# Performance work log

Hardware: AMD Instinct MI355X
Metric: run time of the kernel (lower is better)

Reference implementation:

```python
import jax, jax.numpy as jnp
import numpy as np

DIM = 768
NUM_HEADS = 12
HEAD_DIM = DIM // NUM_HEADS
SCALE = HEAD_DIM ** (-0.5)
WH, WW = 14, 14
NUM_EXTRA = 1
NUM_REL_DIST = (2 * WH - 1) * (2 * WW - 1) + NUM_EXTRA * (NUM_EXTRA + 2)  # 732
N_TOK = WH * WW + NUM_EXTRA  # 197
BATCH = 64


def make_rel_pos_index():
    # mirrors the torch buffer construction (meshgrid 'ij')
    coords = np.stack(np.meshgrid(np.arange(WH), np.arange(WW), indexing='ij'))  # [2,Wh,Ww]
    coords_flat = coords.reshape(2, -1)  # [2, Wh*Ww]
    rel = coords_flat[:, :, None] - coords_flat[:, None, :]  # [2, M, M]
    rel = rel.transpose(1, 2, 0).astype(np.int64)  # [M, M, 2]
    rel[:, :, 0] += WH - 1
    rel[:, :, 1] += WW - 1
    rel[:, :, 0] *= 2 * WW - 1
    idx = np.zeros((N_TOK, N_TOK), dtype=np.int64)
    idx[NUM_EXTRA:, NUM_EXTRA:] = rel.sum(-1)
    idx[0, 0:] = NUM_REL_DIST - 3
    idx[0:, 0] = NUM_REL_DIST - 2
    idx[0, 0] = NUM_REL_DIST - 1
    return jnp.asarray(idx, dtype=jnp.int32)


def setup_inputs() -> dict:
    key = jax.random.key(0)
    ks = jax.random.split(key, 7)
    x = jax.random.normal(ks[0], (BATCH, N_TOK, DIM), dtype=jnp.float32)
    qkv_w = jax.random.normal(ks[1], (3 * DIM, DIM), dtype=jnp.float32) * (DIM ** -0.5)
    q_bias = jax.random.normal(ks[2], (DIM,), dtype=jnp.float32) * 0.02
    v_bias = jax.random.normal(ks[3], (DIM,), dtype=jnp.float32) * 0.02
    rpb_table = jax.random.normal(ks[4], (NUM_REL_DIST, NUM_HEADS), dtype=jnp.float32) * 0.02
    proj_w = jax.random.normal(ks[5], (DIM, DIM), dtype=jnp.float32) * (DIM ** -0.5)
    proj_b = jax.random.normal(ks[6], (DIM,), dtype=jnp.float32) * 0.02
    rel_index = make_rel_pos_index()
    return {"x": x, "qkv_w": qkv_w, "q_bias": q_bias, "v_bias": v_bias,
            "rpb_table": rpb_table, "proj_w": proj_w, "proj_b": proj_b,
            "rel_index": rel_index}


def reference(x, qkv_w, q_bias, v_bias, rpb_table, proj_w, proj_b, rel_index):
    B, N, C = x.shape
    # qkv bias: [q_bias, zeros, v_bias]
    qkv_bias = jnp.concatenate([q_bias, jnp.zeros_like(v_bias), v_bias]).astype(x.dtype)
    qkv = x @ qkv_w.T + qkv_bias  # [B,N,3C]
    qkv = qkv.reshape(B, N, 3, NUM_HEADS, HEAD_DIM).transpose(2, 0, 3, 1, 4)  # [3,B,H,N,d]
    q, k, v = qkv[0] * SCALE, qkv[1], qkv[2]
    # fp32 scores, as in the original
    attn = jnp.einsum('bhnd,bhmd->bhnm', q.astype(jnp.float32), k.astype(jnp.float32))
    # relative position bias gather: [N,N,H] -> [H,N,N]
    bias = rpb_table[rel_index.reshape(-1)].reshape(N, N, NUM_HEADS).transpose(2, 0, 1)
    attn = jax.nn.softmax(attn + bias[None].astype(jnp.float32), axis=-1)
    out = jnp.einsum('bhnm,bhmd->bhnd', attn, v.astype(attn.dtype))
    out = out.transpose(0, 2, 1, 3).reshape(B, N, -1).astype(x.dtype)
    return out @ proj_w.T + proj_b
```

## Files before the change

kernel.cpp:

```cpp
#include <hip/hip_runtime.h>
#include <hip/hip_bf16.h>

#define DIM 768
#define NHEADS 12
#define HD 64
#define NTOK 197
#define BATCH 64
#define NTOKENS (BATCH*NTOK)
#define NPAIR (NTOK*NTOK)
#define QK_SCALE_E2 0.18033688011f
#define LOG2E 1.44269504089f
#define CDIM 2304

typedef short bf16x8 __attribute__((ext_vector_type(8)));
typedef float f32x4 __attribute__((ext_vector_type(4)));

#define MFMA(a,b,c) __builtin_amdgcn_mfma_f32_16x16x32_bf16(a,b,c,0,0,0)

__device__ __forceinline__ unsigned short f2bf(float f) {
    union { float f; unsigned u; } v; v.f = f;
    unsigned r = v.u + 0x7FFFu + ((v.u >> 16) & 1u);
    return (unsigned short)(r >> 16);
}

__device__ __forceinline__ float bf2f(unsigned short u) {
    union { unsigned v; float f; } x; x.v = ((unsigned)u) << 16; return x.f;
}

__device__ __forceinline__ float fexp2(float x) {
    float d;
    asm("v_exp_f32 %0, %1" : "=v"(d) : "v"(x));
    return d;
}

__device__ __forceinline__ unsigned cvtpk(float lo, float hi) {
    unsigned d;
    asm("v_cvt_pk_bf16_f32 %0, %1, %2" : "=v"(d) : "v"(lo), "v"(hi));
    return d;
}

__device__ __forceinline__ unsigned vperm(unsigned s0, unsigned s1, unsigned sel) {
    unsigned d;
    asm("v_perm_b32 %0, %1, %2, %3" : "=v"(d) : "v"(s0), "v"(s1), "s"(sel));
    return d;
}

__device__ __forceinline__ void gload16(const unsigned short* g, unsigned short* l) {
    __builtin_amdgcn_global_load_lds(
        (const __attribute__((address_space(1))) void*)g,
        (__attribute__((address_space(3))) void*)l, 16, 0, 0);
}

__device__ __forceinline__ int xcd_swz(int orig, int nwg) {
    int q = nwg >> 3, r = nwg & 7;
    int xcd = orig & 7, idx = orig >> 3;
    return (xcd < r ? xcd * (q + 1) : r * (q + 1) + (xcd - r) * q) + idx;
}

#define NB_X 4728
#define NB_WQ 864
#define NB_WP 288
#define NB_BIAS 1820

__device__ __forceinline__ void cvt8(const float* __restrict__ s,
                                     unsigned short* __restrict__ d, int t, int n8) {
    if (t >= n8) return;
    float4 a = ((const float4*)s)[t * 2], b = ((const float4*)s)[t * 2 + 1];
    union { unsigned short u[8]; bf16x8 v; } p;
    p.u[0] = f2bf(a.x); p.u[1] = f2bf(a.y); p.u[2] = f2bf(a.z); p.u[3] = f2bf(a.w);
    p.u[4] = f2bf(b.x); p.u[5] = f2bf(b.y); p.u[6] = f2bf(b.z); p.u[7] = f2bf(b.w);
    ((bf16x8*)d)[t] = p.v;
}

__global__ __launch_bounds__(256) void prep(
    const float* __restrict__ x, const float* __restrict__ qw,
    const float* __restrict__ pw, const float* __restrict__ rpb,
    const int* __restrict__ rel,
    unsigned short* __restrict__ Xb, unsigned short* __restrict__ Wqb,
    unsigned short* __restrict__ Wpb, unsigned short* __restrict__ biasm)
{
    int bid = blockIdx.x;
    if (bid < NB_X) {
        cvt8(x, Xb, bid * 256 + threadIdx.x, NB_X * 256);
    } else if (bid < NB_X + NB_WQ) {
        cvt8(qw, Wqb, (bid - NB_X) * 256 + threadIdx.x, NB_WQ * 256);
    } else if (bid < NB_X + NB_WQ + NB_WP) {
        cvt8(pw, Wpb, (bid - NB_X - NB_WQ) * 256 + threadIdx.x, NB_WP * 256);
    } else {
        int t = (bid - NB_X - NB_WQ - NB_WP) * 256 + threadIdx.x;
        if (t < NHEADS * NPAIR) {
            int h = t / NPAIR, p = t - h * NPAIR;
            biasm[t] = f2bf(rpb[rel[p] * NHEADS + h] * LOG2E);
        }
    }
}

__global__ __launch_bounds__(256, 2) void gemm_qkv256(
    const unsigned short* __restrict__ Xb, const unsigned short* __restrict__ Wb,
    const float* __restrict__ qbias, const float* __restrict__ vbias,
    unsigned short* __restrict__ QKVb)
{
    __shared__ __attribute__((aligned(16))) unsigned short As[256 * 64];
    __shared__ __attribute__((aligned(16))) unsigned short Bs[128 * 64];
    int tid = threadIdx.x, lane = tid & 63, wid = tid >> 6;
    int wg = xcd_swz(blockIdx.x, 900);
    int bx = wg / 18, by = wg % 18;
    int m0 = bx * 256, n0 = by * 128;
    int wm = (wid >> 1) * 128, wn = (wid & 1) * 64;
    int r15 = lane & 15, hi = lane >> 4, sx = lane & 7;
    int sl0 = hi ^ sx, sl1 = (hi + 4) ^ sx;

    int slot8 = ((lane & 7) ^ (lane >> 3)) * 8;
    unsigned asrc[8];
    #pragma unroll
    for (int i = 0; i < 8; ++i) {
        int row = i * 32 + wid * 8 + (lane >> 3);
        int ar = m0 + row; if (ar >= NTOKENS) ar = NTOKENS - 1;
        asrc[i] = (unsigned)(ar * DIM + slot8);
    }
    unsigned bsrc[4];
    #pragma unroll
    for (int i = 0; i < 4; ++i) {
        int row = i * 32 + wid * 8 + (lane >> 3);
        bsrc[i] = (unsigned)((n0 + row) * DIM + slot8);
    }

    f32x4 acc[8][4];
    #pragma unroll
    for (int i = 0; i < 8; ++i)
        #pragma unroll
        for (int j = 0; j < 4; ++j) acc[i][j] = (f32x4){0.f, 0.f, 0.f, 0.f};

    for (int k0 = 0; k0 < DIM; k0 += 64) {
        __syncthreads();
        #pragma unroll
        for (int i = 0; i < 8; ++i)
            gload16(Xb + asrc[i] + k0, &As[i * 2048 + wid * 512 + lane * 8]);
        #pragma unroll
        for (int i = 0; i < 4; ++i)
            gload16(Wb + bsrc[i] + k0, &Bs[i * 2048 + wid * 512 + lane * 8]);
        __syncthreads();
        #pragma unroll
        for (int ks = 0; ks < 2; ++ks) {
            int so = (ks ? sl1 : sl0) * 8;
            bf16x8 af[8], bw[4];
            #pragma unroll
            for (int i = 0; i < 8; ++i)
                af[i] = *(const bf16x8*)&As[(wm + i * 16 + r15) * 64 + so];
            #pragma unroll
            for (int j = 0; j < 4; ++j)
                bw[j] = *(const bf16x8*)&Bs[(wn + j * 16 + r15) * 64 + so];
            __builtin_amdgcn_s_setprio(1);
            #pragma unroll
            for (int i = 0; i < 8; ++i)
                #pragma unroll
                for (int j = 0; j < 4; ++j)
                    acc[i][j] = MFMA(af[i], bw[j], acc[i][j]);
            __builtin_amdgcn_s_setprio(0);
        }
    }
    __syncthreads();

    unsigned short* reg = &As[wid * 4096];
    int which = n0 / DIM;
    float scl = (which == 0) ? QK_SCALE_E2 : 1.f;
    #pragma unroll
    for (int h = 0; h < 2; ++h) {
        #pragma unroll
        for (int j = 0; j < 4; ++j) {
            int colr = n0 - which * DIM + wn + j * 16 + r15;
            float bv = (which == 0) ? qbias[colr] : (which == 2 ? vbias[colr] : 0.f);
            #pragma unroll
            for (int mi = 0; mi < 4; ++mi) {
                #pragma unroll
                for (int r = 0; r < 4; ++r) {
                    int lr = mi * 16 + hi * 4 + r;
                    int c = j * 16 + r15;
                    reg[lr * 64 + (c ^ (((lr >> 2) & 3) << 4))] =
                        f2bf((acc[h * 4 + mi][j][r] + bv) * scl);
                }
            }
        }
        #pragma unroll
        for (int it = 0; it < 8; ++it) {
            int c = it * 64 + lane;
            int lr = c >> 3, cc = c & 7;
            int row = m0 + wm + h * 64 + lr;
            if (row < NTOKENS) {
                bf16x8 v = *(bf16x8*)&reg[lr * 64 + ((cc * 8) ^ (((lr >> 2) & 3) << 4))];
                *(bf16x8*)(QKVb + (size_t)row * CDIM + n0 + wn + cc * 8) = v;
            }
        }
    }
}

__global__ __launch_bounds__(256, 2) void gemm_proj(
    const unsigned short* __restrict__ Ob, const unsigned short* __restrict__ Wp,
    const float* __restrict__ pbias, float* __restrict__ out)
{
    __shared__ __attribute__((aligned(16))) unsigned short As[128 * 64];
    __shared__ __attribute__((aligned(16))) unsigned short Bs[128 * 64];
    int tid = threadIdx.x, lane = tid & 63, wid = tid >> 6;
    int wg = xcd_swz(blockIdx.x, 594);
    int bx = wg / 6, by = wg % 6;
    int m0 = bx * 128, n0 = by * 128;
    int wm = (wid >> 1) * 64, wn = (wid & 1) * 64;

    size_t abase[4], bbase[4];
    unsigned short *alds[4], *blds[4];
    #pragma unroll
    for (int i = 0; i < 4; ++i) {
        int chunk = i * 4 + wid;
        int row = chunk * 8 + (lane >> 3);
        int slot = (lane & 7) ^ (row & 7);
        int ar = m0 + row; if (ar >= NTOKENS) ar = NTOKENS - 1;
        abase[i] = (size_t)ar * DIM + slot * 8;
        bbase[i] = (size_t)(n0 + row) * DIM + slot * 8;
        alds[i] = &As[chunk * 512];
        blds[i] = &Bs[chunk * 512];
    }
    int r15 = lane & 15, hi = lane >> 4, sx = lane & 7;
    int s0 = (hi ^ sx) * 8, s1 = ((hi + 4) ^ sx) * 8;
    int arow[4], brow[4];
    #pragma unroll
    for (int i = 0; i < 4; ++i) {
        arow[i] = (wm + i * 16 + r15) * 64;
        brow[i] = (wn + i * 16 + r15) * 64;
    }

    f32x4 acc[4][4];
    #pragma unroll
    for (int i = 0; i < 4; ++i)
        #pragma unroll
        for (int j = 0; j < 4; ++j) acc[i][j] = (f32x4){0.f, 0.f, 0.f, 0.f};

    for (int k0 = 0; k0 < DIM; k0 += 64) {
        __syncthreads();
        #pragma unroll
        for (int i = 0; i < 4; ++i) {
            gload16(Ob + abase[i] + k0, alds[i]);
            gload16(Wp + bbase[i] + k0, blds[i]);
        }
        __syncthreads();
        #pragma unroll
        for (int ks = 0; ks < 2; ++ks) {
            int so = ks ? s1 : s0;
            bf16x8 af[4], bwv[4];
            #pragma unroll
            for (int i = 0; i < 4; ++i) af[i] = *(bf16x8*)&As[arow[i] + so];
            #pragma unroll
            for (int j = 0; j < 4; ++j) bwv[j] = *(bf16x8*)&Bs[brow[j] + so];
            __builtin_amdgcn_s_setprio(1);
            #pragma unroll
            for (int i = 0; i < 4; ++i)
                #pragma unroll
                for (int j = 0; j < 4; ++j)
                    acc[i][j] = MFMA(af[i], bwv[j], acc[i][j]);
            __builtin_amdgcn_s_setprio(0);
        }
    }

    #pragma unroll
    for (int j = 0; j < 4; ++j) {
        int col = n0 + wn + j * 16 + r15;
        float bv = pbias[col];
        #pragma unroll
        for (int i = 0; i < 4; ++i) {
            #pragma unroll
            for (int r = 0; r < 4; ++r) {
                int row = m0 + wm + i * 16 + hi * 4 + r;
                if (row < NTOKENS)
                    out[(size_t)row * DIM + col] = acc[i][j][r] + bv;
            }
        }
    }
}

#define KP 72
#define PP 232
#define VPITCH 256

__global__ __launch_bounds__(256, 2) void attn(
    const unsigned short* __restrict__ QKV, const unsigned short* __restrict__ biasm,
    unsigned short* __restrict__ O)
{
    __shared__ __attribute__((aligned(16))) unsigned short VT[64 * VPITCH];
    __shared__ __attribute__((aligned(16))) unsigned short KlPl[208 * KP];

    int tid = threadIdx.x, lane = tid & 63, wid = tid >> 6;
    int r15 = lane & 15, hi = lane >> 4;
    int wg = blockIdx.x;
    int g = wg >> 5, qt = (wg >> 3) & 3, p = wg & 7;
    int bh = g * 8 + p;
    int h = bh % NHEADS, b = bh / NHEADS;
    size_t tb = (size_t)b * NTOK;
    int hq = h * 64;
    int rbase = qt * 64 + wid * 16 + hi * 4;

    int kcol = (tid & 7) * 8;
    bf16x8 kreg[7];
    #pragma unroll
    for (int t = 0; t < 7; ++t) {
        int row = t * 32 + (tid >> 3);
        int rc = row < NTOK ? row : (NTOK - 1);
        kreg[t] = *(const bf16x8*)(QKV + (tb + rc) * CDIM + 768 + hq + kcol);
    }

    bf16x8 v0r[4], v1r[4];
    #pragma unroll
    for (int it = 0; it < 4; ++it) {
        int c = it * 256 + tid;
        int rp = c >> 3, kc = c & 7;
        int r0 = 2 * rp, r1 = 2 * rp + 1;
        bf16x8 z = (bf16x8)(short)0;
        v0r[it] = z; v1r[it] = z;
        if (r0 < NTOK) v0r[it] = *(const bf16x8*)(QKV + (tb + r0) * CDIM + 1536 + hq + kc * 8);
        if (r1 < NTOK) v1r[it] = *(const bf16x8*)(QKV + (tb + r1) * CDIM + 1536 + hq + kc * 8);
    }

    int qrow_g = qt * 64 + wid * 16 + r15;
    int qsrc = qrow_g < NTOK ? qrow_g : (NTOK - 1);
    bf16x8 aq[2];
    #pragma unroll
    for (int ks = 0; ks < 2; ++ks)
        aq[ks] = *(const bf16x8*)(QKV + (tb + qsrc) * CDIM + hq + ks * 32 + hi * 8);

    unsigned short breg[4][13];
    {
        const unsigned short* bb = biasm + h * NPAIR;
        #pragma unroll
        for (int r = 0; r < 4; ++r) {
            int row_g = rbase + r;
            int rowc = row_g < NTOK ? row_g : (NTOK - 1);
            const unsigned short* brow = bb + rowc * NTOK + r15;
            #pragma unroll
            for (int t = 0; t < 13; ++t) {
                int off = t * 16;
                if (t == 12 && r15 >= 5) off = 0;
                breg[r][t] = brow[off];
            }
        }
    }

    #pragma unroll
    for (int t = 0; t < 7; ++t) {
        int row = t * 32 + (tid >> 3);
        if (row < NTOK)
            *(bf16x8*)&KlPl[row * KP + kcol] = kreg[t];
    }

    #pragma unroll
    for (int it = 0; it < 4; ++it) {
        int c = it * 256 + tid;
        int rp = c >> 3, kc = c & 7;
        if (rp < 112) {
            union { bf16x8 v; unsigned u[4]; } a0, a1;
            a0.v = v0r[it]; a1.v = v1r[it];
            #pragma unroll
            for (int rr = 0; rr < 4; ++rr) {
                unsigned we = vperm(a1.u[rr], a0.u[rr], 0x05040100u);
                unsigned wo = vperm(a1.u[rr], a0.u[rr], 0x07060302u);
                int j0 = 2 * rr, j1 = 2 * rr + 1;
                int s20 = (rp >> 2) ^ j0 ^ kc;
                int s21 = (rp >> 2) ^ j1 ^ kc;
                *(unsigned*)&VT[(kc * 8 + j0) * VPITCH + s20 * 8 + (rp & 3) * 2] = we;
                *(unsigned*)&VT[(kc * 8 + j1) * VPITCH + s21 * 8 + (rp & 3) * 2] = wo;
            }
        }
    }
    __syncthreads();

    f32x4 sa[13];
    #pragma unroll
    for (int t = 0; t < 13; ++t) sa[t] = (f32x4){0.f,0.f,0.f,0.f};
    __builtin_amdgcn_s_setprio(1);
    #pragma unroll
    for (int t = 0; t < 13; ++t) {
        #pragma unroll
        for (int ks = 0; ks < 2; ++ks) {
            bf16x8 bk = *(bf16x8*)&KlPl[(t * 16 + r15) * KP + ks * 32 + hi * 8];
            sa[t] = MFMA(aq[ks], bk, sa[t]);
        }
    }
    __builtin_amdgcn_s_setprio(0);
    __syncthreads();

    int plbase = wid * (16 * PP);
    float invr[4];
    #pragma unroll
    for (int r = 0; r < 4; ++r) {
        #pragma unroll
        for (int t = 0; t < 13; ++t) {
            int col = t * 16 + r15;
            if (col < NTOK) sa[t][r] += bf2f(breg[r][t]);
            else            sa[t][r] = -1e30f;
        }
        float m0a = fmaxf(fmaxf(sa[0][r], sa[1][r]), fmaxf(sa[2][r], sa[3][r]));
        float m1a = fmaxf(fmaxf(sa[4][r], sa[5][r]), fmaxf(sa[6][r], sa[7][r]));
        float m2a = fmaxf(fmaxf(sa[8][r], sa[9][r]), fmaxf(sa[10][r], sa[11][r]));
        float mx = fmaxf(fmaxf(m0a, m1a), fmaxf(m2a, sa[12][r]));
        #pragma unroll
        for (int m = 1; m < 16; m <<= 1) mx = fmaxf(mx, __shfl_xor(mx, m));
        #pragma unroll
        for (int t = 0; t < 13; ++t)
            sa[t][r] = fexp2(sa[t][r] - mx);
        float s0a = (sa[0][r] + sa[1][r]) + (sa[2][r] + sa[3][r]);
        float s1a = (sa[4][r] + sa[5][r]) + (sa[6][r] + sa[7][r]);
        float s2a = (sa[8][r] + sa[9][r]) + (sa[10][r] + sa[11][r]);
        float sum = (s0a + s1a) + (s2a + sa[12][r]);
        int roff = plbase + (hi * 4 + r) * PP;
        #pragma unroll
        for (int tp = 0; tp < 6; ++tp) {
            unsigned u = cvtpk(sa[2 * tp][r], sa[2 * tp + 1][r]);
            KlPl[roff + (2 * tp) * 16 + r15] = (unsigned short)u;
            KlPl[roff + (2 * tp + 1) * 16 + r15] = (unsigned short)(u >> 16);
        }
        KlPl[roff + 192 + r15] = f2bf(sa[12][r]);
        KlPl[roff + 208 + r15] = 0;
        #pragma unroll
        for (int m = 1; m < 16; m <<= 1) sum += __shfl_xor(sum, m);
        invr[r] = __builtin_amdgcn_rcpf(sum);
    }

    f32x4 oa[4];
    #pragma unroll
    for (int dt = 0; dt < 4; ++dt) oa[dt] = (f32x4){0.f,0.f,0.f,0.f};
    int X = hi ^ (r15 & 7) ^ (r15 >> 3);
    __builtin_amdgcn_s_setprio(1);
    #pragma unroll
    for (int ks = 0; ks < 7; ++ks) {
        bf16x8 ap = *(bf16x8*)&KlPl[plbase + r15 * PP + ks * 32 + hi * 8];
        #pragma unroll
        for (int dt = 0; dt < 4; ++dt) {
            int d = dt * 16 + r15;
            int slotp = (ks * 4) ^ (dt * 2) ^ X;
            bf16x8 bv = *(bf16x8*)&VT[d * VPITCH + slotp * 8];
            oa[dt] = MFMA(ap, bv, oa[dt]);
        }
    }
    __builtin_amdgcn_s_setprio(0);

    #pragma unroll
    for (int r = 0; r < 4; ++r) {
        int roff = plbase + (hi * 4 + r) * 72;
        #pragma unroll
        for (int dp = 0; dp < 2; ++dp) {
            unsigned u = cvtpk(oa[2 * dp][r] * invr[r], oa[2 * dp + 1][r] * invr[r]);
            KlPl[roff + (2 * dp) * 16 + r15] = (unsigned short)u;
            KlPl[roff + (2 * dp + 1) * 16 + r15] = (unsigned short)(u >> 16);
        }
    }
    #pragma unroll
    for (int it = 0; it < 2; ++it) {
        int c = it * 64 + lane;
        int lr = c >> 3, cc = c & 7;
        int qrow = qt * 64 + wid * 16 + lr;
        if (qrow < NTOK)
            *(bf16x8*)(O + (tb + qrow) * DIM + hq + cc * 8) =
                *(bf16x8*)&KlPl[plbase + lr * 72 + cc * 8];
    }
}

extern "C" void kernel_launch(void* const* d_in, const int* in_sizes, int n_in,
                              void* d_out, int out_size, void* d_ws, size_t ws_size,
                              hipStream_t stream) {
    const float* x      = (const float*)d_in[0];
    const float* qkv_w  = (const float*)d_in[1];
    const float* q_bias = (const float*)d_in[2];
    const float* v_bias = (const float*)d_in[3];
    const float* rpb    = (const float*)d_in[4];
    const float* proj_w = (const float*)d_in[5];
    const float* proj_b = (const float*)d_in[6];
    const int*   rel    = (const int*)d_in[7];
    float* out = (float*)d_out;

    const size_t NELEM = (size_t)NTOKENS * DIM;
    const size_t WQKV  = (size_t)3 * DIM * DIM;
    const size_t WPROJ = (size_t)DIM * DIM;
    unsigned short* Xb   = (unsigned short*)d_ws;
    unsigned short* Wqb  = Xb + NELEM;
    unsigned short* Wpb  = Wqb + WQKV;
    unsigned short* QKVb = Wpb + WPROJ;
    unsigned short* biasm = QKVb + (size_t)NTOKENS * CDIM;
    unsigned short* Ob = Xb;

    prep<<<NB_X + NB_WQ + NB_WP + NB_BIAS, 256, 0, stream>>>(
        x, qkv_w, proj_w, rpb, rel, Xb, Wqb, Wpb, biasm);

    gemm_qkv256<<<900, 256, 0, stream>>>(Xb, Wqb, q_bias, v_bias, QKVb);

    attn<<<3072, 256, 0, stream>>>(QKVb, biasm, Ob);

    gemm_proj<<<594, 256, 0, stream>>>(Ob, Wpb, proj_b, out);
}
```

Measured before the change: 137.9 us.

## Fold the nearly empty fourth query tile into wave 3 of the third tile

Each (batch, head) pair previously used four 64-row query tiles, and the last tile held only 5 valid rows out of 197. The grid now uses three tiles per pair, and wave 3 of tile 2 also processes query rows 192-196 as a second pass: a second QK^T, then softmax, PV and the output write via a shared macro. This cuts the number of workgroups by a quarter and avoids reloading K/V and rebuilding the transposed V tile for the mostly padded tile. In exchange one wave per workgroup does double work, which creates tail imbalance, and the extra sa2 accumulators add register pressure.

```diff
diff --git a/kernel.cpp b/kernel.cpp
--- a/kernel.cpp
+++ b/kernel.cpp
@@ -280,6 +280,78 @@
 #define PP 232
 #define VPITCH 256
 
+#define SM_PV_OUT(SA, BREG, TB0) do {                                          \
+    float invr_[4];                                                            \
+    _Pragma("unroll")                                                          \
+    for (int r = 0; r < 4; ++r) {                                              \
+        _Pragma("unroll")                                                      \
+        for (int t = 0; t < 13; ++t) {                                         \
+            int col = t * 16 + r15;                                            \
+            if (col < NTOK) SA[t][r] += bf2f(BREG[r][t]);                      \
+            else            SA[t][r] = -1e30f;                                 \
+        }                                                                      \
+        float m0a = fmaxf(fmaxf(SA[0][r], SA[1][r]), fmaxf(SA[2][r], SA[3][r]));\
+        float m1a = fmaxf(fmaxf(SA[4][r], SA[5][r]), fmaxf(SA[6][r], SA[7][r]));\
+        float m2a = fmaxf(fmaxf(SA[8][r], SA[9][r]), fmaxf(SA[10][r], SA[11][r]));\
+        float mx = fmaxf(fmaxf(m0a, m1a), fmaxf(m2a, SA[12][r]));              \
+        _Pragma("unroll")                                                      \
+        for (int m = 1; m < 16; m <<= 1) mx = fmaxf(mx, __shfl_xor(mx, m));    \
+        _Pragma("unroll")                                                      \
+        for (int t = 0; t < 13; ++t) SA[t][r] = fexp2(SA[t][r] - mx);          \
+        float s0a = (SA[0][r] + SA[1][r]) + (SA[2][r] + SA[3][r]);             \
+        float s1a = (SA[4][r] + SA[5][r]) + (SA[6][r] + SA[7][r]);             \
+        float s2a = (SA[8][r] + SA[9][r]) + (SA[10][r] + SA[11][r]);           \
+        float sum = (s0a + s1a) + (s2a + SA[12][r]);                           \
+        int roff = plbase + (hi * 4 + r) * PP;                                 \
+        _Pragma("unroll")                                                      \
+        for (int tp = 0; tp < 6; ++tp) {                                       \
+            unsigned u = cvtpk(SA[2 * tp][r], SA[2 * tp + 1][r]);              \
+            KlPl[roff + (2 * tp) * 16 + r15] = (unsigned short)u;              \
+            KlPl[roff + (2 * tp + 1) * 16 + r15] = (unsigned short)(u >> 16);  \
+        }                                                                      \
+        KlPl[roff + 192 + r15] = f2bf(SA[12][r]);                              \
+        KlPl[roff + 208 + r15] = 0;                                            \
+        _Pragma("unroll")                                                      \
+        for (int m = 1; m < 16; m <<= 1) sum += __shfl_xor(sum, m);            \
+        invr_[r] = __builtin_amdgcn_rcpf(sum);                                 \
+    }                                                                          \
+    f32x4 oa[4];                                                               \
+    _Pragma("unroll")                                                          \
+    for (int dt = 0; dt < 4; ++dt) oa[dt] = (f32x4){0.f,0.f,0.f,0.f};          \
+    __builtin_amdgcn_s_setprio(1);                                             \
+    _Pragma("unroll")                                                          \
+    for (int ks = 0; ks < 7; ++ks) {                                           \
+        bf16x8 ap = *(bf16x8*)&KlPl[plbase + r15 * PP + ks * 32 + hi * 8];     \
+        _Pragma("unroll")                                                      \
+        for (int dt = 0; dt < 4; ++dt) {                                       \
+            int d = dt * 16 + r15;                                             \
+            int slotp = (ks * 4) ^ (dt * 2) ^ X;                               \
+            bf16x8 bv = *(bf16x8*)&VT[d * VPITCH + slotp * 8];                 \
+            oa[dt] = MFMA(ap, bv, oa[dt]);                                     \
+        }                                                                      \
+    }                                                                          \
+    __builtin_amdgcn_s_setprio(0);                                             \
+    _Pragma("unroll")                                                          \
+    for (int r = 0; r < 4; ++r) {                                              \
+        int roff = plbase + (hi * 4 + r) * 72;                                 \
+        _Pragma("unroll")                                                      \
+        for (int dp = 0; dp < 2; ++dp) {                                       \
+            unsigned u = cvtpk(oa[2 * dp][r] * invr_[r], oa[2 * dp + 1][r] * invr_[r]); \
+            KlPl[roff + (2 * dp) * 16 + r15] = (unsigned short)u;              \
+            KlPl[roff + (2 * dp + 1) * 16 + r15] = (unsigned short)(u >> 16);  \
+        }                                                                      \
+    }                                                                          \
+    _Pragma("unroll")                                                          \
+    for (int it = 0; it < 2; ++it) {                                           \
+        int c = it * 64 + lane;                                                \
+        int lr = c >> 3, cc = c & 7;                                           \
+        int qrow = (TB0) + lr;                                                 \
+        if (qrow < NTOK)                                                       \
+            *(bf16x8*)(O + (tb + qrow) * DIM + hq + cc * 8) =                  \
+                *(bf16x8*)&KlPl[plbase + lr * 72 + cc * 8];                    \
+    }                                                                          \
+} while (0)
+
 __global__ __launch_bounds__(256, 2) void attn(
     const unsigned short* __restrict__ QKV, const unsigned short* __restrict__ biasm,
     unsigned short* __restrict__ O)
@@ -290,12 +362,13 @@
     int tid = threadIdx.x, lane = tid & 63, wid = tid >> 6;
     int r15 = lane & 15, hi = lane >> 4;
     int wg = blockIdx.x;
-    int g = wg >> 5, qt = (wg >> 3) & 3, p = wg & 7;
+    int g = wg / 24, rem = wg % 24, qt = rem >> 3, p = rem & 7;
     int bh = g * 8 + p;
     int h = bh % NHEADS, b = bh / NHEADS;
     size_t tb = (size_t)b * NTOK;
     int hq = h * 64;
     int rbase = qt * 64 + wid * 16 + hi * 4;
+    bool dbl = (qt == 2) && (wid == 3);
 
     int kcol = (tid & 7) * 8;
     bf16x8 kreg[7];
@@ -320,10 +393,16 @@
 
     int qrow_g = qt * 64 + wid * 16 + r15;
     int qsrc = qrow_g < NTOK ? qrow_g : (NTOK - 1);
-    bf16x8 aq[2];
+    bf16x8 aq[2], aq2[2];
     #pragma unroll
     for (int ks = 0; ks < 2; ++ks)
         aq[ks] = *(const bf16x8*)(QKV + (tb + qsrc) * CDIM + hq + ks * 32 + hi * 8);
+    if (dbl) {
+        int q2 = 192 + r15; if (q2 > NTOK - 1) q2 = NTOK - 1;
+        #pragma unroll
+        for (int ks = 0; ks < 2; ++ks)
+            aq2[ks] = *(const bf16x8*)(QKV + (tb + q2) * CDIM + hq + ks * 32 + hi * 8);
+    }
 
     unsigned short breg[4][13];
     {
@@ -370,7 +449,7 @@
     }
     __syncthreads();
 
-    f32x4 sa[13];
+    f32x4 sa[13], sa2[13];
     #pragma unroll
     for (int t = 0; t < 13; ++t) sa[t] = (f32x4){0.f,0.f,0.f,0.f};
     __builtin_amdgcn_s_setprio(1);
@@ -383,81 +462,41 @@
         }
     }
     __builtin_amdgcn_s_setprio(0);
+    if (dbl) {
+        #pragma unroll
+        for (int t = 0; t < 13; ++t) sa2[t] = (f32x4){0.f,0.f,0.f,0.f};
+        #pragma unroll
+        for (int t = 0; t < 13; ++t) {
+            #pragma unroll
+            for (int ks = 0; ks < 2; ++ks) {
+                bf16x8 bk = *(bf16x8*)&KlPl[(t * 16 + r15) * KP + ks * 32 + hi * 8];
+                sa2[t] = MFMA(aq2[ks], bk, sa2[t]);
+            }
+        }
+    }
     __syncthreads();
 
     int plbase = wid * (16 * PP);
-    float invr[4];
-    #pragma unroll
-    for (int r = 0; r < 4; ++r) {
-        #pragma unroll
-        for (int t = 0; t < 13; ++t) {
-            int col = t * 16 + r15;
-            if (col < NTOK) sa[t][r] += bf2f(breg[r][t]);
-            else            sa[t][r] = -1e30f;
-        }
-        float m0a = fmaxf(fmaxf(sa[0][r], sa[1][r]), fmaxf(sa[2][r], sa[3][r]));
-        float m1a = fmaxf(fmaxf(sa[4][r], sa[5][r]), fmaxf(sa[6][r], sa[7][r]));
-        float m2a = fmaxf(fmaxf(sa[8][r], sa[9][r]), fmaxf(sa[10][r], sa[11][r]));
-        float mx = fmaxf(fmaxf(m0a, m1a), fmaxf(m2a, sa[12][r]));
-        #pragma unroll
-        for (int m = 1; m < 16; m <<= 1) mx = fmaxf(mx, __shfl_xor(mx, m));
-        #pragma unroll
-        for (int t = 0; t < 13; ++t)
-            sa[t][r] = fexp2(sa[t][r] - mx);
-        float s0a = (sa[0][r] + sa[1][r]) + (sa[2][r] + sa[3][r]);
-        float s1a = (sa[4][r] + sa[5][r]) + (sa[6][r] + sa[7][r]);
-        float s2a = (sa[8][r] + sa[9][r]) + (sa[10][r] + sa[11][r]);
-        float sum = (s0a + s1a) + (s2a + sa[12][r]);
-        int roff = plbase + (hi * 4 + r) * PP;
-        #pragma unroll
-        for (int tp = 0; tp < 6; ++tp) {
-            unsigned u = cvtpk(sa[2 * tp][r], sa[2 * tp + 1][r]);
-            KlPl[roff + (2 * tp) * 16 + r15] = (unsigned short)u;
-            KlPl[roff + (2 * tp + 1) * 16 + r15] = (unsigned short)(u >> 16);
-        }
-        KlPl[roff + 192 + r15] = f2bf(sa[12][r]);
-        KlPl[roff + 208 + r15] = 0;
-        #pragma unroll
-        for (int m = 1; m < 16; m <<= 1) sum += __shfl_xor(sum, m);
-        invr[r] = __builtin_amdgcn_rcpf(sum);
-    }
-
-    f32x4 oa[4];
-    #pragma unroll
-    for (int dt = 0; dt < 4; ++dt) oa[dt] = (f32x4){0.f,0.f,0.f,0.f};
     int X = hi ^ (r15 & 7) ^ (r15 >> 3);
-    __builtin_amdgcn_s_setprio(1);
-    #pragma unroll
-    for (int ks = 0; ks < 7; ++ks) {
-        bf16x8 ap = *(bf16x8*)&KlPl[plbase + r15 * PP + ks * 32 + hi * 8];
-        #pragma unroll
-        for (int dt = 0; dt < 4; ++dt) {
-            int d = dt * 16 + r15;
-            int slotp = (ks * 4) ^ (dt * 2) ^ X;
-            bf16x8 bv = *(bf16x8*)&VT[d * VPITCH + slotp * 8];
-            oa[dt] = MFMA(ap, bv, oa[dt]);
-        }
-    }
-    __builtin_amdgcn_s_setprio(0);
-
-    #pragma unroll
-    for (int r = 0; r < 4; ++r) {
-        int roff = plbase + (hi * 4 + r) * 72;
-        #pragma unroll
-        for (int dp = 0; dp < 2; ++dp) {
-            unsigned u = cvtpk(oa[2 * dp][r] * invr[r], oa[2 * dp + 1][r] * invr[r]);
-            KlPl[roff + (2 * dp) * 16 + r15] = (unsigned short)u;
-            KlPl[roff + (2 * dp + 1) * 16 + r15] = (unsigned short)(u >> 16);
-        }
-    }
-    #pragma unroll
-    for (int it = 0; it < 2; ++it) {
-        int c = it * 64 + lane;
-        int lr = c >> 3, cc = c & 7;
-        int qrow = qt * 64 + wid * 16 + lr;
-        if (qrow < NTOK)
-            *(bf16x8*)(O + (tb + qrow) * DIM + hq + cc * 8) =
-                *(bf16x8*)&KlPl[plbase + lr * 72 + cc * 8];
+
+    SM_PV_OUT(sa, breg, qt * 64 + wid * 16);
+
+    if (dbl) {
+        unsigned short breg2[4][13];
+        const unsigned short* bb = biasm + h * NPAIR;
+        #pragma unroll
+        for (int r = 0; r < 4; ++r) {
+            int row_g = 192 + hi * 4 + r;
+            int rowc = row_g < NTOK ? row_g : (NTOK - 1);
+            const unsigned short* brow = bb + rowc * NTOK + r15;
+            #pragma unroll
+            for (int t = 0; t < 13; ++t) {
+                int off = t * 16;
+                if (t == 12 && r15 >= 5) off = 0;
+                breg2[r][t] = brow[off];
+            }
+        }
+        SM_PV_OUT(sa2, breg2, 192);
     }
 }
 
@@ -489,7 +528,7 @@
 
     gemm_qkv256<<<900, 256, 0, stream>>>(Xb, Wqb, q_bias, v_bias, QKVb);
 
-    attn<<<3072, 256, 0, stream>>>(QKVb, biasm, Ob);
+    attn<<<2304, 256, 0, stream>>>(QKVb, biasm, Ob);
 
     gemm_proj<<<594, 256, 0, stream>>>(Ob, Wpb, proj_b, out);
 }
```

Result: slower. 141.9 us (+2.9%).
